# Kernel tuning notes

Measured on AMD Instinct MI355X. Metric: run time of the kernel, lower is better.

## Reference

```python
import jax, jax.numpy as jnp
import numpy as np

B, C, H, W = 16, 64, 128, 128
K = 3
Z = 128


def setup_inputs() -> dict:
    key = jax.random.key(0)
    k1, k2, k3, k4 = jax.random.split(key, 4)
    x = jax.random.normal(k1, (B, C, H, W), dtype=jnp.float32)
    z = jax.random.normal(k2, (B, Z), dtype=jnp.float32)
    # generator: Linear(Z -> C*C*K*K), scaled for stable conv outputs
    gen_w = jax.random.normal(k3, (Z, C * C * K * K), dtype=jnp.float32) * 0.02
    gen_b = jax.random.normal(k4, (C * C * K * K,), dtype=jnp.float32) * 0.02
    return {"x": x, "z": z, "gen_w": gen_w, "gen_b": gen_b}


def _conv_one(xi, wi):
    # xi: [C,H,W], wi: [C_out,C_in,K,K]; 'same' padding conv, no bias
    out = jax.lax.conv_general_dilated(
        xi[None], wi, window_strides=(1, 1), padding="SAME",
        dimension_numbers=("NCHW", "OIHW", "NCHW"))
    return out[0]


def reference(x, z, gen_w, gen_b):
    # per-sample weight generation: [B, C*C*K*K] -> [B, C, C, K, K]
    weight = (z @ gen_w + gen_b).reshape(B, C, C, K, K)
    # batched per-sample convolution (replaces the python loop over batch)
    return jax.vmap(_conv_one)(x, weight)
```

## Files before the change

### kernel.cpp

```cpp
#include <hip/hip_runtime.h>
#include <hip/hip_bf16.h>

typedef __attribute__((ext_vector_type(4))) float f32x4;
typedef __attribute__((ext_vector_type(8))) short short8;

#define B_ 16
#define C_ 64
#define H_ 128
#define W_ 128
#define Z_ 128
#define HW_ (H_*W_)
#define IDXN (C_*C_*9)
#define NT 18

__device__ __forceinline__ unsigned short f2bf(float f) {
  __hip_bfloat16 h = __float2bfloat16(f);
  return *reinterpret_cast<unsigned short*>(&h);
}

__global__ __launch_bounds__(256) void wgen_k(
    const float* __restrict__ z, const float* __restrict__ gw,
    const float* __restrict__ gb, unsigned short* __restrict__ wfrag) {
  __shared__ __align__(16) float zs[B_*Z_];
  int t = threadIdx.x;
#pragma unroll
  for (int i = 0; i < 8; ++i) zs[i*256 + t] = z[i*256 + t];
  __syncthreads();
  int lane = t & 63, bg = t >> 6;
  int b0 = bg*4;
  int idx0 = blockIdx.x*128 + lane;
  float acc[4][2];
  float bv0 = gb[idx0], bv1 = gb[idx0 + 64];
#pragma unroll
  for (int bi = 0; bi < 4; ++bi) { acc[bi][0] = bv0; acc[bi][1] = bv1; }

  for (int z0 = 0; z0 < Z_; z0 += 4) {
    float ga[4], gbv[4];
#pragma unroll
    for (int zi = 0; zi < 4; ++zi) {
      ga[zi]  = gw[(size_t)(z0+zi)*IDXN + idx0];
      gbv[zi] = gw[(size_t)(z0+zi)*IDXN + idx0 + 64];
    }
#pragma unroll
    for (int bi = 0; bi < 4; ++bi) {
      f32x4 zq = *reinterpret_cast<const f32x4*>(&zs[(b0+bi)*Z_ + z0]);
      acc[bi][0] = fmaf(zq[0], ga[0], fmaf(zq[1], ga[1], fmaf(zq[2], ga[2], fmaf(zq[3], ga[3], acc[bi][0]))));
      acc[bi][1] = fmaf(zq[0], gbv[0], fmaf(zq[1], gbv[1], fmaf(zq[2], gbv[2], fmaf(zq[3], gbv[3], acc[bi][1]))));
    }
  }
#pragma unroll
  for (int ni = 0; ni < 2; ++ni) {
    int idx = idx0 + ni*64;
    int kw = idx % 3, r1 = idx/3;
    int kh = r1 % 3, r2 = r1/3;
    int ci = r2 & 63, co = r2 >> 6;
    int k = (kh*3 + kw)*C_ + ci;
    int ts = k >> 5, kin = k & 31;
    int lm = (co & 15) | ((kin >> 3) << 4);
    int j = kin & 7, m = co >> 4;
    int base = ((ts*4 + m)*64 + lm)*8 + j;
#pragma unroll
    for (int bi = 0; bi < 4; ++bi)
      wfrag[(size_t)(b0+bi)*(NT*4*64*8) + base] = f2bf(acc[bi][ni]);
  }
}

__global__ __launch_bounds__(512, 4) void conv_k(
    const float* __restrict__ x,
    const unsigned short* __restrict__ wfrag,
    float* __restrict__ out) {
  __shared__ __align__(16) unsigned char xs[4*130*128];
  int orig = blockIdx.x;
  int blk = (orig & 7)*128 + (orig >> 3);
  int b = blk >> 6;
  int h0 = (blk & 63)*2;
  int tid = threadIdx.x;
  int v = tid >> 6, lane = tid & 63;

  {
    int r = v >> 1, hf = v & 1;
    int hh = h0 - 1 + r;
    bool hv = (hh >= 0) & (hh < H_);
    unsigned char* ldsrow = xs + r*(130*128);
    if (hv) {
      if (lane < 8) {
        int s = hf ? (1032 + lane) : lane;
        uint4 zv; zv.x = 0; zv.y = 0; zv.z = 0; zv.w = 0;
        *reinterpret_cast<uint4*>(ldsrow + s*16) = zv;
      }
      const float* xrow = x + (((size_t)b*C_)*H_ + hh)*W_;
      int w0 = 2*lane, col0 = w0 + 1, col1 = w0 + 2;
      int g = lane >> 3;
#pragma unroll
      for (int i = 0; i < 4; ++i) {
        int chunk = (hf*4 + i + g) & 7;
        float2 v2[8];
#pragma unroll
        for (int j = 0; j < 8; ++j)
          v2[j] = *reinterpret_cast<const float2*>(xrow + (size_t)(chunk*8 + j)*HW_ + w0);
        uint4 o0, o1;
        unsigned short* s0 = reinterpret_cast<unsigned short*>(&o0);
        unsigned short* s1 = reinterpret_cast<unsigned short*>(&o1);
#pragma unroll
        for (int j = 0; j < 8; ++j) { s0[j] = f2bf(v2[j].x); s1[j] = f2bf(v2[j].y); }
        int a0 = col0*128 + (((chunk ^ col0) & 7) << 4);
        int a1 = col1*128 + (((chunk ^ col1) & 7) << 4);
        *reinterpret_cast<uint4*>(ldsrow + a0) = o0;
        *reinterpret_cast<uint4*>(ldsrow + a1) = o1;
      }
    } else {
      uint4 zv; zv.x = 0; zv.y = 0; zv.z = 0; zv.w = 0;
#pragma unroll
      for (int it = 0; it < 9; ++it) {
        int di = it*64 + lane;
        if (di < 520) *reinterpret_cast<uint4*>(ldsrow + (hf*520 + di)*16) = zv;
      }
    }
  }

  int l15 = lane & 15, lhi = lane >> 4;
  int phr = v >> 2, pw0 = ((v >> 1) & 1)*64;
  int mt0 = (v & 1)*2;
  const unsigned short* wb = wfrag + (size_t)b*(NT*4*64*8);

  short8 wf0 = *reinterpret_cast<const short8*>(wb + (((mt0 + 0)*64 + lane)*8));
  short8 wf1 = *reinterpret_cast<const short8*>(wb + (((mt0 + 1)*64 + lane)*8));

  __syncthreads();

  f32x4 acc[4][2];
#pragma unroll
  for (int mp = 0; mp < 4; ++mp)
#pragma unroll
    for (int nc = 0; nc < 2; ++nc)
      acc[mp][nc] = (f32x4){0.f, 0.f, 0.f, 0.f};

#pragma unroll
  for (int t = 0; t < NT; ++t) {
    int kk = t >> 1, kh = kk/3, kw = kk - 3*kh, half = t & 1;
    short8 nf0, nf1;
    if (t + 1 < NT) {
      nf0 = *reinterpret_cast<const short8*>(wb + ((((t+1)*4 + mt0 + 0)*64 + lane)*8));
      nf1 = *reinterpret_cast<const short8*>(wb + ((((t+1)*4 + mt0 + 1)*64 + lane)*8));
    }
    int chunk = half*4 + lhi;
    short8 xa[4];
#pragma unroll
    for (int mp = 0; mp < 4; ++mp) {
      int col = pw0 + mp*16 + l15 + kw;
      int addr = ((phr + kh)*130 + col)*128 + (((chunk ^ col) & 7) << 4);
      xa[mp] = *reinterpret_cast<const short8*>(&xs[addr]);
    }
#pragma unroll
    for (int mp = 0; mp < 4; ++mp) {
      acc[mp][0] = __builtin_amdgcn_mfma_f32_16x16x32_bf16(xa[mp], wf0, acc[mp][0], 0, 0, 0);
      acc[mp][1] = __builtin_amdgcn_mfma_f32_16x16x32_bf16(xa[mp], wf1, acc[mp][1], 0, 0, 0);
    }
    wf0 = nf0; wf1 = nf1;
  }

  __syncthreads();
  float* obuf = reinterpret_cast<float*>(xs);
#pragma unroll
  for (int nc = 0; nc < 2; ++nc) {
    int co = (mt0 + nc)*16 + l15;
#pragma unroll
    for (int mp = 0; mp < 4; ++mp) {
      int px = pw0 + mp*16 + lhi*4;
      *reinterpret_cast<f32x4*>(&obuf[co*260 + phr*128 + px]) = acc[mp][nc];
    }
  }
  __syncthreads();
  {
    float* ob = out + ((size_t)b*C_)*HW_ + (size_t)h0*W_;
#pragma unroll
    for (int i = 0; i < 8; ++i) {
      int co = i*8 + v;
      f32x4 val = *reinterpret_cast<const f32x4*>(&obuf[co*260 + lane*4]);
      *reinterpret_cast<f32x4*>(ob + (size_t)co*HW_ + lane*4) = val;
    }
  }
}

__global__ void sentinel_k(float* out, int n) {
  int i = blockIdx.x*256 + threadIdx.x;
  if (i < n) out[i] = 1.0e6f;
}

extern "C" void kernel_launch(void* const* d_in, const int* in_sizes, int n_in,
                              void* d_out, int out_size, void* d_ws, size_t ws_size,
                              hipStream_t stream) {
  const float* x  = (const float*)d_in[0];
  const float* z  = (const float*)d_in[1];
  const float* gw = (const float*)d_in[2];
  const float* gb = (const float*)d_in[3];
  float* out = (float*)d_out;

  size_t wfrag_elems = (size_t)B_*IDXN;
  size_t need = wfrag_elems*sizeof(unsigned short);
  if (ws_size < need) {
    sentinel_k<<<(out_size + 255)/256, 256, 0, stream>>>(out, out_size);
    return;
  }
  unsigned short* wfrag = (unsigned short*)d_ws;

  wgen_k <<<IDXN/128, 256, 0, stream>>>(z, gw, gb, wfrag);
  conv_k <<<B_*(H_/2), 512, 0, stream>>>(x, wfrag, out);
}
```

Baseline: 52.09 us.

## Process eight output rows per block with a ring-buffered, prefetched input halo

Each conv block now computes eight output rows in four passes of two rows, keeping a six-row circular LDS buffer so halo rows are reused between passes rather than reloaded. Global loads for the next row pair are issued before the MFMA loop and written to LDS after it, overlapping memory latency with compute. Output goes straight from registers to global memory instead of through an LDS transpose. The grid shrinks to 256 blocks with lower occupancy (launch bounds 2), which risks underfilling the GPU. The uncoalesced 16-byte direct stores may also cost bandwidth.

```diff
diff --git a/kernel.cpp b/kernel.cpp
--- a/kernel.cpp
+++ b/kernel.cpp
@@ -65,120 +65,150 @@
   }
 }
 
-__global__ __launch_bounds__(512, 4) void conv_k(
+__global__ __launch_bounds__(512, 2) void conv_k(
     const float* __restrict__ x,
     const unsigned short* __restrict__ wfrag,
     float* __restrict__ out) {
-  __shared__ __align__(16) unsigned char xs[4*130*128];
+  __shared__ __align__(16) unsigned char xs[6*130*128];
   int orig = blockIdx.x;
-  int blk = (orig & 7)*128 + (orig >> 3);
-  int b = blk >> 6;
-  int h0 = (blk & 63)*2;
+  int blk = (orig & 7)*32 + (orig >> 3);
+  int b = blk >> 4;
+  int hbase = (blk & 15)*8;
   int tid = threadIdx.x;
   int v = tid >> 6, lane = tid & 63;
-
-  {
-    int r = v >> 1, hf = v & 1;
-    int hh = h0 - 1 + r;
-    bool hv = (hh >= 0) & (hh < H_);
-    unsigned char* ldsrow = xs + r*(130*128);
-    if (hv) {
-      if (lane < 8) {
-        int s = hf ? (1032 + lane) : lane;
-        uint4 zv; zv.x = 0; zv.y = 0; zv.z = 0; zv.w = 0;
-        *reinterpret_cast<uint4*>(ldsrow + s*16) = zv;
-      }
-      const float* xrow = x + (((size_t)b*C_)*H_ + hh)*W_;
-      int w0 = 2*lane, col0 = w0 + 1, col1 = w0 + 2;
-      int g = lane >> 3;
-#pragma unroll
-      for (int i = 0; i < 4; ++i) {
-        int chunk = (hf*4 + i + g) & 7;
-        float2 v2[8];
-#pragma unroll
-        for (int j = 0; j < 8; ++j)
-          v2[j] = *reinterpret_cast<const float2*>(xrow + (size_t)(chunk*8 + j)*HW_ + w0);
-        uint4 o0, o1;
-        unsigned short* s0 = reinterpret_cast<unsigned short*>(&o0);
-        unsigned short* s1 = reinterpret_cast<unsigned short*>(&o1);
-#pragma unroll
-        for (int j = 0; j < 8; ++j) { s0[j] = f2bf(v2[j].x); s1[j] = f2bf(v2[j].y); }
-        int a0 = col0*128 + (((chunk ^ col0) & 7) << 4);
-        int a1 = col1*128 + (((chunk ^ col1) & 7) << 4);
-        *reinterpret_cast<uint4*>(ldsrow + a0) = o0;
-        *reinterpret_cast<uint4*>(ldsrow + a1) = o1;
-      }
-    } else {
-      uint4 zv; zv.x = 0; zv.y = 0; zv.z = 0; zv.w = 0;
-#pragma unroll
-      for (int it = 0; it < 9; ++it) {
-        int di = it*64 + lane;
-        if (di < 520) *reinterpret_cast<uint4*>(ldsrow + (hf*520 + di)*16) = zv;
-      }
-    }
-  }
-
   int l15 = lane & 15, lhi = lane >> 4;
+
+  int sr = v >> 2;
+  int hq = v & 3;
+  int g = lane >> 3;
+  int w0 = 2*lane, col0 = w0 + 1, col1 = w0 + 2;
+  const float* xb = x + ((size_t)b*C_)*HW_;
   int phr = v >> 2, pw0 = ((v >> 1) & 1)*64;
   int mt0 = (v & 1)*2;
   const unsigned short* wb = wfrag + (size_t)b*(NT*4*64*8);
 
+  if (tid < 96) {
+    int sl = tid >> 4, cc = (tid >> 3) & 1, ch = tid & 7;
+    int col = cc ? 129 : 0;
+    uint4 zv; zv.x = 0; zv.y = 0; zv.z = 0; zv.w = 0;
+    *reinterpret_cast<uint4*>(&xs[(sl*130 + col)*128 + ch*16]) = zv;
+  }
+
+  float2 sv[2][8];
+
+  auto stage_direct = [&](int gbase, int slbase) {
+    int grow = gbase + sr;
+    bool valid = (grow >= 0) & (grow < H_);
+    int gc = min(max(grow, 0), H_-1);
+    const float* xrow = xb + (size_t)gc*W_;
+    int sl = slbase + sr;
+#pragma unroll
+    for (int i = 0; i < 2; ++i) {
+      int chunk = (hq*2 + i + g) & 7;
+      uint4 o0, o1;
+      unsigned short* s0 = reinterpret_cast<unsigned short*>(&o0);
+      unsigned short* s1 = reinterpret_cast<unsigned short*>(&o1);
+#pragma unroll
+      for (int j = 0; j < 8; ++j) {
+        float2 f = *reinterpret_cast<const float2*>(xrow + (size_t)(chunk*8 + j)*HW_ + w0);
+        s0[j] = valid ? f2bf(f.x) : (unsigned short)0;
+        s1[j] = valid ? f2bf(f.y) : (unsigned short)0;
+      }
+      *reinterpret_cast<uint4*>(&xs[(sl*130 + col0)*128 + (((chunk ^ col0) & 7) << 4)]) = o0;
+      *reinterpret_cast<uint4*>(&xs[(sl*130 + col1)*128 + (((chunk ^ col1) & 7) << 4)]) = o1;
+    }
+  };
+  auto stage_issue = [&](int gbase) {
+    int grow = gbase + sr;
+    int gc = min(max(grow, 0), H_-1);
+    const float* xrow = xb + (size_t)gc*W_;
+#pragma unroll
+    for (int i = 0; i < 2; ++i) {
+      int chunk = (hq*2 + i + g) & 7;
+#pragma unroll
+      for (int j = 0; j < 8; ++j)
+        sv[i][j] = *reinterpret_cast<const float2*>(xrow + (size_t)(chunk*8 + j)*HW_ + w0);
+    }
+  };
+  auto stage_commit = [&](int gbase, int slbase6) {
+    int grow = gbase + sr;
+    bool valid = (grow >= 0) & (grow < H_);
+    int sl = slbase6 + sr; if (sl >= 6) sl -= 6;
+#pragma unroll
+    for (int i = 0; i < 2; ++i) {
+      int chunk = (hq*2 + i + g) & 7;
+      uint4 o0, o1;
+      unsigned short* s0 = reinterpret_cast<unsigned short*>(&o0);
+      unsigned short* s1 = reinterpret_cast<unsigned short*>(&o1);
+#pragma unroll
+      for (int j = 0; j < 8; ++j) {
+        s0[j] = valid ? f2bf(sv[i][j].x) : (unsigned short)0;
+        s1[j] = valid ? f2bf(sv[i][j].y) : (unsigned short)0;
+      }
+      *reinterpret_cast<uint4*>(&xs[(sl*130 + col0)*128 + (((chunk ^ col0) & 7) << 4)]) = o0;
+      *reinterpret_cast<uint4*>(&xs[(sl*130 + col1)*128 + (((chunk ^ col1) & 7) << 4)]) = o1;
+    }
+  };
+
+  stage_direct(hbase - 1, 0);
+  stage_direct(hbase + 1, 2);
+
   short8 wf0 = *reinterpret_cast<const short8*>(wb + (((mt0 + 0)*64 + lane)*8));
   short8 wf1 = *reinterpret_cast<const short8*>(wb + (((mt0 + 1)*64 + lane)*8));
-
   __syncthreads();
 
-  f32x4 acc[4][2];
-#pragma unroll
-  for (int mp = 0; mp < 4; ++mp)
-#pragma unroll
-    for (int nc = 0; nc < 2; ++nc)
-      acc[mp][nc] = (f32x4){0.f, 0.f, 0.f, 0.f};
-
-#pragma unroll
-  for (int t = 0; t < NT; ++t) {
-    int kk = t >> 1, kh = kk/3, kw = kk - 3*kh, half = t & 1;
-    short8 nf0, nf1;
-    if (t + 1 < NT) {
-      nf0 = *reinterpret_cast<const short8*>(wb + ((((t+1)*4 + mt0 + 0)*64 + lane)*8));
-      nf1 = *reinterpret_cast<const short8*>(wb + ((((t+1)*4 + mt0 + 1)*64 + lane)*8));
-    }
-    int chunk = half*4 + lhi;
-    short8 xa[4];
-#pragma unroll
-    for (int mp = 0; mp < 4; ++mp) {
-      int col = pw0 + mp*16 + l15 + kw;
-      int addr = ((phr + kh)*130 + col)*128 + (((chunk ^ col) & 7) << 4);
-      xa[mp] = *reinterpret_cast<const short8*>(&xs[addr]);
-    }
-#pragma unroll
-    for (int mp = 0; mp < 4; ++mp) {
-      acc[mp][0] = __builtin_amdgcn_mfma_f32_16x16x32_bf16(xa[mp], wf0, acc[mp][0], 0, 0, 0);
-      acc[mp][1] = __builtin_amdgcn_mfma_f32_16x16x32_bf16(xa[mp], wf1, acc[mp][1], 0, 0, 0);
-    }
-    wf0 = nf0; wf1 = nf1;
-  }
-
-  __syncthreads();
-  float* obuf = reinterpret_cast<float*>(xs);
-#pragma unroll
-  for (int nc = 0; nc < 2; ++nc) {
-    int co = (mt0 + nc)*16 + l15;
-#pragma unroll
-    for (int mp = 0; mp < 4; ++mp) {
-      int px = pw0 + mp*16 + lhi*4;
-      *reinterpret_cast<f32x4*>(&obuf[co*260 + phr*128 + px]) = acc[mp][nc];
-    }
-  }
-  __syncthreads();
-  {
-    float* ob = out + ((size_t)b*C_)*HW_ + (size_t)h0*W_;
-#pragma unroll
-    for (int i = 0; i < 8; ++i) {
-      int co = i*8 + v;
-      f32x4 val = *reinterpret_cast<const f32x4*>(&obuf[co*260 + lane*4]);
-      *reinterpret_cast<f32x4*>(ob + (size_t)co*HW_ + lane*4) = val;
-    }
+#pragma unroll 1
+  for (int p = 0; p < 4; ++p) {
+    if (p < 3) stage_issue(hbase + 2*p + 3);
+
+    f32x4 acc[4][2];
+#pragma unroll
+    for (int mp = 0; mp < 4; ++mp)
+#pragma unroll
+      for (int nc = 0; nc < 2; ++nc)
+        acc[mp][nc] = (f32x4){0.f, 0.f, 0.f, 0.f};
+
+    int rsb = 2*p + phr;
+#pragma unroll
+    for (int t = 0; t < NT; ++t) {
+      int kk = t >> 1, kh = kk/3, kw = kk - 3*kh, half = t & 1;
+      short8 nf0, nf1;
+      if (t + 1 < NT) {
+        nf0 = *reinterpret_cast<const short8*>(wb + ((((t+1)*4 + mt0 + 0)*64 + lane)*8));
+        nf1 = *reinterpret_cast<const short8*>(wb + ((((t+1)*4 + mt0 + 1)*64 + lane)*8));
+      }
+      int chunk = half*4 + lhi;
+      int rs = rsb + kh; if (rs >= 6) rs -= 6;
+      short8 xa[4];
+#pragma unroll
+      for (int mp = 0; mp < 4; ++mp) {
+        int col = pw0 + mp*16 + l15 + kw;
+        xa[mp] = *reinterpret_cast<const short8*>(&xs[(rs*130 + col)*128 + (((chunk ^ col) & 7) << 4)]);
+      }
+#pragma unroll
+      for (int mp = 0; mp < 4; ++mp) {
+        acc[mp][0] = __builtin_amdgcn_mfma_f32_16x16x32_bf16(xa[mp], wf0, acc[mp][0], 0, 0, 0);
+        acc[mp][1] = __builtin_amdgcn_mfma_f32_16x16x32_bf16(xa[mp], wf1, acc[mp][1], 0, 0, 0);
+      }
+      wf0 = nf0; wf1 = nf1;
+    }
+
+    int ph = hbase + 2*p + phr;
+#pragma unroll
+    for (int nc = 0; nc < 2; ++nc) {
+      int co = (mt0 + nc)*16 + l15;
+      float* op = out + (((size_t)b*C_ + co)*H_ + ph)*W_;
+#pragma unroll
+      for (int mp = 0; mp < 4; ++mp)
+        *reinterpret_cast<f32x4*>(op + pw0 + mp*16 + lhi*4) = acc[mp][nc];
+    }
+
+    if (p < 3) {
+      stage_commit(hbase + 2*p + 3, (2*p + 4) % 6);
+      wf0 = *reinterpret_cast<const short8*>(wb + (((mt0 + 0)*64 + lane)*8));
+      wf1 = *reinterpret_cast<const short8*>(wb + (((mt0 + 1)*64 + lane)*8));
+    }
+    __syncthreads();
   }
 }
 
@@ -205,5 +235,5 @@
   unsigned short* wfrag = (unsigned short*)d_ws;
 
   wgen_k <<<IDXN/128, 256, 0, stream>>>(z, gw, gb, wfrag);
-  conv_k <<<B_*(H_/2), 512, 0, stream>>>(x, wfrag, out);
-}
+  conv_k <<<B_*16, 512, 0, stream>>>(x, wfrag, out);
+}
```

After: 50.57 us. -2.9%, faster.
